# Kernel optimization log

Measured on AMD Instinct MI355X. Metric: run time of the kernel, lower is better.

The kernel has to match this reference:

```python
import jax, jax.numpy as jnp
import numpy as np


def _gcn(x, src, dst, W, b, n):
    # PyG GCNConv: out = D^-1/2 (A+I) D^-1/2 (x @ W) + b, deg includes self-loop
    xw = x @ W
    ones = jnp.ones(src.shape[0], x.dtype)
    deg = jax.ops.segment_sum(ones, dst, num_segments=n) + 1.0
    dinv = jax.lax.rsqrt(deg)
    norm = (dinv[src] * dinv[dst])[:, None]
    agg = jax.ops.segment_sum(xw[src] * norm, dst, num_segments=n)
    agg = agg + xw / deg[:, None]  # self-loop term: norm = 1/deg
    return agg + b


def _bn(x, g, b, m, v, eps=1e-5):
    # BatchNorm1d eval mode with running stats
    return (x - m) * jax.lax.rsqrt(v + eps) * g + b


def setup_inputs() -> dict:
    key = jax.random.key(0)
    ks = jax.random.split(key, 32)
    N, E, G, F, H, D, L, EM = 500000, 2500000, 10000, 64, 64, 128, 10, 160000
    s = 0.05
    inp = {
        'x': jax.random.normal(ks[0], (N, F), jnp.float32),
        'edge_index': jax.random.randint(ks[1], (2, E), 0, N),
        'batch': jnp.sort(jax.random.randint(ks[2], (N,), 0, G)),
        'macro_edges': jax.random.randint(ks[3], (2, EM), 0, G),
        'G': G,
        'W1': jax.random.normal(ks[4], (F, H)) * s, 'b1': jnp.zeros((H,)),
        'W2': jax.random.normal(ks[5], (H, H)) * s, 'b2': jnp.zeros((H,)),
        'FW1': jax.random.normal(ks[6], (H, D)) * s, 'Fb1': jnp.zeros((D,)),
        'FW2': jax.random.normal(ks[7], (D, L)) * s, 'Fb2': jnp.zeros((L,)),
        'MW1': jax.random.normal(ks[8], (D, D)) * s, 'mb1': jnp.zeros((D,)),
        'g1': jnp.ones((D,)), 'be1': jnp.zeros((D,)),
        'm1': jnp.zeros((D,)), 'v1': jnp.ones((D,)),
        'MW2': jax.random.normal(ks[9], (D, D)) * s, 'mb2': jnp.zeros((D,)),
        'g2': jnp.ones((D,)), 'be2': jnp.zeros((D,)),
        'm2': jnp.zeros((D,)), 'v2': jnp.ones((D,)),
        'MW3': jax.random.normal(ks[10], (D, L)) * s, 'mb3': jnp.zeros((L,)),
    }
    return inp


def reference(x, edge_index, batch, macro_edges, G,
              W1, b1, W2, b2, FW1, Fb1, FW2, Fb2,
              MW1, mb1, g1, be1, m1, v1,
              MW2, mb2, g2, be2, m2, v2,
              MW3, mb3):
    n = x.shape[0]
    src, dst = edge_index[0], edge_index[1]
    # SAGE (graph-level model), eval mode => dropout is identity
    h1 = jax.nn.relu(_gcn(x, src, dst, W1, b1, n))
    h2 = jax.nn.relu(_gcn(h1, src, dst, W2, b2, n))
    a1 = h2 @ FW1 + Fb1
    sums = jax.ops.segment_sum(a1, batch, num_segments=G)
    cnt = jax.ops.segment_sum(jnp.ones(n, x.dtype), batch, num_segments=G)
    loc = sums / jnp.maximum(cnt, 1.0)[:, None]        # [G, 128] graph embeddings
    ic = loc @ FW2 + Fb2                                # [G, L]
    # SuperMacroGCN over macro graph
    ms, md = macro_edges[0], macro_edges[1]
    z = jax.nn.relu(_bn(_gcn(loc, ms, md, MW1, mb1, G), g1, be1, m1, v1))
    z = jax.nn.relu(_bn(_gcn(z, ms, md, MW2, mb2, G), g2, be2, m2, v2))
    glob = z
    hc = _gcn(glob, ms, md, MW3, mb3, G)
    return (hc, ic, loc, glob, jnp.float32(0.0))
```

## Files before the change

kernel.cpp:

```cpp
#include <hip/hip_runtime.h>
#include <hip/hip_fp16.h>


typedef float nf4 __attribute__((ext_vector_type(4)));
typedef _Float16 v4h __attribute__((ext_vector_type(4)));
typedef float v4f __attribute__((ext_vector_type(4)));
struct __align__(8) h4 { __half2 a, b; };

__global__ void hist_kernel(const int* __restrict__ dst, int* __restrict__ hist, int E) {
    int e = blockIdx.x * blockDim.x + threadIdx.x;
    if (e < E) atomicAdd(&hist[dst[e]], 1);
}

__global__ void finalize_deg(const int* __restrict__ hist, float* __restrict__ dinv,
                             float* __restrict__ drecip, int n) {
    int i = blockIdx.x * blockDim.x + threadIdx.x;
    if (i < n) {
        float c = (float)hist[i] + 1.0f;
        dinv[i]   = rsqrtf(c);
        drecip[i] = 1.0f / c;
    }
}

__global__ __launch_bounds__(256) void scan1(const int* __restrict__ cnt, int* __restrict__ pre,
                                             int* __restrict__ bsum, int n) {
    __shared__ int s[256];
    int base = blockIdx.x * 1024;
    int t = threadIdx.x;
    int v[4];
    int loc = 0;
#pragma unroll
    for (int j = 0; j < 4; j++) {
        int i = base + t * 4 + j;
        v[j] = (i < n) ? cnt[i] : 0;
        loc += v[j];
    }
    s[t] = loc;
    __syncthreads();
    for (int off = 1; off < 256; off <<= 1) {
        int x = (t >= off) ? s[t - off] : 0;
        __syncthreads();
        s[t] += x;
        __syncthreads();
    }
    int run = s[t] - loc;
    if (t == 255) bsum[blockIdx.x] = s[255];
#pragma unroll
    for (int j = 0; j < 4; j++) {
        int i = base + t * 4 + j;
        if (i < n) pre[i] = run;
        run += v[j];
    }
}

__global__ __launch_bounds__(512) void scan2(int* __restrict__ bsum, int nb) {
    __shared__ int s[512];
    int t = threadIdx.x;
    int v = (t < nb) ? bsum[t] : 0;
    s[t] = v;
    __syncthreads();
    for (int off = 1; off < 512; off <<= 1) {
        int x = (t >= off) ? s[t - off] : 0;
        __syncthreads();
        s[t] += x;
        __syncthreads();
    }
    if (t < nb) bsum[t] = s[t] - v;
}

__global__ void scan3(int* __restrict__ pre, const int* __restrict__ bsum,
                      int* __restrict__ cursor, int n, int E) {
    int i = blockIdx.x * blockDim.x + threadIdx.x;
    if (i < n) {
        int v = pre[i] + bsum[i >> 10];
        pre[i] = v;
        cursor[i] = v;
    }
    if (i == 0) pre[n] = E;
}

__global__ __launch_bounds__(256) void scatter_xcd(const int* __restrict__ src,
                                                   const int* __restrict__ dst,
                                                   int* __restrict__ cursor,
                                                   int* __restrict__ col,
                                                   int E, int per_chunk, int npx) {
    int bucket = blockIdx.x & 7;
    int chunk  = blockIdx.x >> 3;
    int lo = bucket * npx;
    int hi = lo + npx;
    int e0 = chunk * per_chunk;
    int e1 = min(e0 + per_chunk, E);
    for (int e = e0 + threadIdx.x; e < e1; e += 256) {
        int d = dst[e];
        if (d < lo || d >= hi) continue;
        int p = atomicAdd(&cursor[d], 1);
        col[p] = src[e];
    }
}

__global__ void scatter_kernel(const int* __restrict__ src, const int* __restrict__ dst,
                               int* __restrict__ cursor, int* __restrict__ col, int E) {
    int e = blockIdx.x * blockDim.x + threadIdx.x;
    if (e >= E) return;
    int p = atomicAdd(&cursor[dst[e]], 1);
    col[p] = src[e];
}

__global__ __launch_bounds__(256) void csr_agg_bn128(const int* __restrict__ rowptr,
                                                     const int* __restrict__ col,
                                                     const float* __restrict__ A,
                                                     const float* __restrict__ bias,
                                                     const float* __restrict__ dinv,
                                                     const float* __restrict__ gam,
                                                     const float* __restrict__ bet,
                                                     const float* __restrict__ mean,
                                                     const float* __restrict__ var,
                                                     float* __restrict__ Z, int N) {
    constexpr int F = 128, TPN = 32, NPB = 8;
    int node = blockIdx.x * NPB + threadIdx.x / TPN;
    int lane = threadIdx.x % TPN;
    if (node >= N) return;
    int c = lane * 4;
    float4 acc = *(const float4*)&A[(size_t)node * F + c];
    int e0 = rowptr[node], e1 = rowptr[node + 1];
    int e = e0;
    for (; e + 4 <= e1; e += 4) {
        int s0 = col[e + 0], s1 = col[e + 1], s2 = col[e + 2], s3 = col[e + 3];
        float4 v0 = *(const float4*)&A[(size_t)s0 * F + c];
        float4 v1 = *(const float4*)&A[(size_t)s1 * F + c];
        float4 v2 = *(const float4*)&A[(size_t)s2 * F + c];
        float4 v3 = *(const float4*)&A[(size_t)s3 * F + c];
        acc.x += v0.x + v1.x + v2.x + v3.x;
        acc.y += v0.y + v1.y + v2.y + v3.y;
        acc.z += v0.z + v1.z + v2.z + v3.z;
        acc.w += v0.w + v1.w + v2.w + v3.w;
    }
    for (; e < e1; e++) {
        int s = col[e];
        float4 v = *(const float4*)&A[(size_t)s * F + c];
        acc.x += v.x; acc.y += v.y; acc.z += v.z; acc.w += v.w;
    }
    float dv = dinv[node];
    float4 b4 = *(const float4*)&bias[c];
    float4 g4 = *(const float4*)&gam[c];
    float4 be4 = *(const float4*)&bet[c];
    float4 m4 = *(const float4*)&mean[c];
    float4 v4 = *(const float4*)&var[c];
    float4 o;
    o.x = fmaxf((acc.x * dv + b4.x - m4.x) * rsqrtf(v4.x + 1e-5f) * g4.x + be4.x, 0.f);
    o.y = fmaxf((acc.y * dv + b4.y - m4.y) * rsqrtf(v4.y + 1e-5f) * g4.y + be4.y, 0.f);
    o.z = fmaxf((acc.z * dv + b4.z - m4.z) * rsqrtf(v4.z + 1e-5f) * g4.z + be4.z, 0.f);
    o.w = fmaxf((acc.w * dv + b4.w - m4.w) * rsqrtf(v4.w + 1e-5f) * g4.w + be4.w, 0.f);
    *(float4*)&Z[(size_t)node * F + c] = o;
}

__global__ __launch_bounds__(256) void gemm_n64(const float* __restrict__ X,
                                                const float* __restrict__ W,
                                                const float* __restrict__ dinv,
                                                __half* __restrict__ XW, int N) {
    __shared__ float Xs[64][68];
    const int tid = threadIdx.x;
    const int tc = tid & 15;
    const int tr = tid >> 4;
    const int r0 = blockIdx.x * 64;

#pragma unroll
    for (int p = 0; p < 4; p++) {
        int row = p * 16 + (tid >> 4);
        int col = (tid & 15) * 4;
        float4 v = make_float4(0.f, 0.f, 0.f, 0.f);
        if (r0 + row < N) {
            nf4 nv = __builtin_nontemporal_load((const nf4*)&X[(size_t)(r0 + row) * 64 + col]);
            v = make_float4(nv.x, nv.y, nv.z, nv.w);
        }
        *(float4*)&Xs[row][col] = v;
    }
    __syncthreads();

    float acc[4][4];
#pragma unroll
    for (int i = 0; i < 4; i++)
#pragma unroll
        for (int j = 0; j < 4; j++) acc[i][j] = 0.f;

    const float* wp = W + tc * 4;
#pragma unroll 8
    for (int k = 0; k < 64; k++) {
        float4 wv = *(const float4*)&wp[k * 64];
        float x0 = Xs[tr * 4 + 0][k];
        float x1 = Xs[tr * 4 + 1][k];
        float x2 = Xs[tr * 4 + 2][k];
        float x3 = Xs[tr * 4 + 3][k];
        acc[0][0] += x0 * wv.x; acc[0][1] += x0 * wv.y; acc[0][2] += x0 * wv.z; acc[0][3] += x0 * wv.w;
        acc[1][0] += x1 * wv.x; acc[1][1] += x1 * wv.y; acc[1][2] += x1 * wv.z; acc[1][3] += x1 * wv.w;
        acc[2][0] += x2 * wv.x; acc[2][1] += x2 * wv.y; acc[2][2] += x2 * wv.z; acc[2][3] += x2 * wv.w;
        acc[3][0] += x3 * wv.x; acc[3][1] += x3 * wv.y; acc[3][2] += x3 * wv.z; acc[3][3] += x3 * wv.w;
    }

#pragma unroll
    for (int i = 0; i < 4; i++) {
        int row = r0 + tr * 4 + i;
        if (row >= N) continue;
        float dv = dinv[row];
        h4 o;
        o.a = __floats2half2_rn(acc[i][0] * dv, acc[i][1] * dv);
        o.b = __floats2half2_rn(acc[i][2] * dv, acc[i][3] * dv);
        *(h4*)&XW[(size_t)row * 64 + tc * 4] = o;
    }
}

__global__ __launch_bounds__(256) void gemm_agg_n64(const int* __restrict__ rowptr,
                                                    const int* __restrict__ col,
                                                    const __half* __restrict__ A,
                                                    const float* __restrict__ b_prev,
                                                    const float* __restrict__ W,
                                                    const float* __restrict__ dinv,
                                                    __half* __restrict__ XW, int N) {
    __shared__ _Float16 Xh[64][68];
    __shared__ _Float16 WhT[64][68];
    const int tid = threadIdx.x;
    const int r0 = blockIdx.x * 64;

    for (int i = tid; i < 4096; i += 256) {
        int k = i >> 6, c = i & 63;
        WhT[c][k] = (_Float16)W[i];
    }

#pragma unroll
    for (int p = 0; p < 4; p++) {
        int row = p * 16 + (tid >> 4);
        int node = r0 + row;
        int c = (tid & 15) * 4;
        float4 acc = make_float4(0.f, 0.f, 0.f, 0.f);
        if (node < N) {
            h4 sv = *(const h4*)&A[(size_t)node * 64 + c];
            float2 f0 = __half22float2(sv.a);
            float2 f1 = __half22float2(sv.b);
            acc = make_float4(f0.x, f0.y, f1.x, f1.y);
            int e0 = rowptr[node], e1 = rowptr[node + 1];
            int e = e0;
            for (; e + 4 <= e1; e += 4) {
                int s0 = col[e + 0], s1 = col[e + 1], s2 = col[e + 2], s3 = col[e + 3];
                h4 v0 = *(const h4*)&A[(size_t)s0 * 64 + c];
                h4 v1 = *(const h4*)&A[(size_t)s1 * 64 + c];
                h4 v2 = *(const h4*)&A[(size_t)s2 * 64 + c];
                h4 v3 = *(const h4*)&A[(size_t)s3 * 64 + c];
                float2 a0 = __half22float2(v0.a), b0 = __half22float2(v0.b);
                float2 a1 = __half22float2(v1.a), b1 = __half22float2(v1.b);
                float2 a2 = __half22float2(v2.a), b2 = __half22float2(v2.b);
                float2 a3 = __half22float2(v3.a), b3 = __half22float2(v3.b);
                acc.x += a0.x + a1.x + a2.x + a3.x;
                acc.y += a0.y + a1.y + a2.y + a3.y;
                acc.z += b0.x + b1.x + b2.x + b3.x;
                acc.w += b0.y + b1.y + b2.y + b3.y;
            }
            for (; e < e1; e++) {
                int s = col[e];
                h4 v = *(const h4*)&A[(size_t)s * 64 + c];
                float2 a = __half22float2(v.a), b = __half22float2(v.b);
                acc.x += a.x; acc.y += a.y; acc.z += b.x; acc.w += b.y;
            }
            float dv = dinv[node];
            float4 b4 = *(const float4*)&b_prev[c];
            acc.x = fmaxf(acc.x * dv + b4.x, 0.f);
            acc.y = fmaxf(acc.y * dv + b4.y, 0.f);
            acc.z = fmaxf(acc.z * dv + b4.z, 0.f);
            acc.w = fmaxf(acc.w * dv + b4.w, 0.f);
        }
        v4h o;
        o.x = (_Float16)acc.x; o.y = (_Float16)acc.y;
        o.z = (_Float16)acc.z; o.w = (_Float16)acc.w;
        *(v4h*)&Xh[row][c] = o;
    }
    __syncthreads();

    const int wv = tid >> 6;
    const int lane = tid & 63;
    const int lr = lane & 15;
    const int kg = lane >> 4;

    v4f acc0 = {0.f, 0.f, 0.f, 0.f};
    v4f acc1 = {0.f, 0.f, 0.f, 0.f};
    v4f acc2 = {0.f, 0.f, 0.f, 0.f};
    v4f acc3 = {0.f, 0.f, 0.f, 0.f};
#pragma unroll
    for (int s = 0; s < 4; s++) {
        v4h af = *(const v4h*)&Xh[wv * 16 + lr][s * 16 + kg * 4];
        v4h bf0 = *(const v4h*)&WhT[0 * 16 + lr][s * 16 + kg * 4];
        v4h bf1 = *(const v4h*)&WhT[1 * 16 + lr][s * 16 + kg * 4];
        v4h bf2 = *(const v4h*)&WhT[2 * 16 + lr][s * 16 + kg * 4];
        v4h bf3 = *(const v4h*)&WhT[3 * 16 + lr][s * 16 + kg * 4];
        acc0 = __builtin_amdgcn_mfma_f32_16x16x16f16(af, bf0, acc0, 0, 0, 0);
        acc1 = __builtin_amdgcn_mfma_f32_16x16x16f16(af, bf1, acc1, 0, 0, 0);
        acc2 = __builtin_amdgcn_mfma_f32_16x16x16f16(af, bf2, acc2, 0, 0, 0);
        acc3 = __builtin_amdgcn_mfma_f32_16x16x16f16(af, bf3, acc3, 0, 0, 0);
    }

#pragma unroll
    for (int j = 0; j < 4; j++) {
        int row = r0 + wv * 16 + kg * 4 + j;
        if (row >= N) continue;
        float dv = dinv[row];
        XW[(size_t)row * 64 +  0 + lr] = (__half)(acc0[j] * dv);
        XW[(size_t)row * 64 + 16 + lr] = (__half)(acc1[j] * dv);
        XW[(size_t)row * 64 + 32 + lr] = (__half)(acc2[j] * dv);
        XW[(size_t)row * 64 + 48 + lr] = (__half)(acc3[j] * dv);
    }
}

__global__ __launch_bounds__(128) void segmean_agg(const int* __restrict__ rowptr,
                                                   const int* __restrict__ col,
                                                   const __half* __restrict__ A2,
                                                   const float* __restrict__ b2,
                                                   const float* __restrict__ dinv,
                                                   const int* __restrict__ batch,
                                                   float* __restrict__ M,
                                                   float* __restrict__ bscale,
                                                   int N, int G) {
    int g = blockIdx.x * 2 + (threadIdx.x >> 6);
    if (g >= G) return;
    int lane = threadIdx.x & 15;
    int sub  = (threadIdx.x >> 4) & 3;
    int c = lane * 4;

    int lo = 0, hi = N;
    while (lo < hi) { int m = (lo + hi) >> 1; if (batch[m] < g) lo = m + 1; else hi = m; }
    int start = lo;
    hi = N;
    while (lo < hi) { int m = (lo + hi) >> 1; if (batch[m] < g + 1) lo = m + 1; else hi = m; }
    int end = lo;

    float4 b4 = *(const float4*)&b2[c];
    float4 msum = make_float4(0.f, 0.f, 0.f, 0.f);

    for (int node = start + sub; node < end; node += 4) {
        h4 sv = *(const h4*)&A2[(size_t)node * 64 + c];
        float2 f0 = __half22float2(sv.a);
        float2 f1 = __half22float2(sv.b);
        float4 acc = make_float4(f0.x, f0.y, f1.x, f1.y);
        int e0 = rowptr[node], e1 = rowptr[node + 1];
        int e = e0;
        for (; e + 4 <= e1; e += 4) {
            int s0 = col[e + 0], s1 = col[e + 1], s2 = col[e + 2], s3 = col[e + 3];
            h4 v0 = *(const h4*)&A2[(size_t)s0 * 64 + c];
            h4 v1 = *(const h4*)&A2[(size_t)s1 * 64 + c];
            h4 v2 = *(const h4*)&A2[(size_t)s2 * 64 + c];
            h4 v3 = *(const h4*)&A2[(size_t)s3 * 64 + c];
            float2 a0 = __half22float2(v0.a), q0 = __half22float2(v0.b);
            float2 a1 = __half22float2(v1.a), q1 = __half22float2(v1.b);
            float2 a2 = __half22float2(v2.a), q2 = __half22float2(v2.b);
            float2 a3 = __half22float2(v3.a), q3 = __half22float2(v3.b);
            acc.x += a0.x + a1.x + a2.x + a3.x;
            acc.y += a0.y + a1.y + a2.y + a3.y;
            acc.z += q0.x + q1.x + q2.x + q3.x;
            acc.w += q0.y + q1.y + q2.y + q3.y;
        }
        for (; e < e1; e++) {
            int s = col[e];
            h4 v = *(const h4*)&A2[(size_t)s * 64 + c];
            float2 a = __half22float2(v.a), q = __half22float2(v.b);
            acc.x += a.x; acc.y += a.y; acc.z += q.x; acc.w += q.y;
        }
        float dv = dinv[node];
        msum.x += fmaxf(acc.x * dv + b4.x, 0.f);
        msum.y += fmaxf(acc.y * dv + b4.y, 0.f);
        msum.z += fmaxf(acc.z * dv + b4.z, 0.f);
        msum.w += fmaxf(acc.w * dv + b4.w, 0.f);
    }

    msum.x += __shfl_xor(msum.x, 16); msum.y += __shfl_xor(msum.y, 16);
    msum.z += __shfl_xor(msum.z, 16); msum.w += __shfl_xor(msum.w, 16);
    msum.x += __shfl_xor(msum.x, 32); msum.y += __shfl_xor(msum.y, 32);
    msum.z += __shfl_xor(msum.z, 32); msum.w += __shfl_xor(msum.w, 32);

    int cnt = end - start;
    float inv = (cnt > 0) ? 1.f / (float)cnt : 0.f;
    if (sub == 0) {
        float4 o;
        o.x = msum.x * inv; o.y = msum.y * inv;
        o.z = msum.z * inv; o.w = msum.w * inv;
        *(float4*)&M[(size_t)g * 64 + c] = o;
        if (lane == 0) bscale[g] = (cnt > 0) ? 1.f : 0.f;
    }
}

__global__ __launch_bounds__(256) void loc_gemm(const float* __restrict__ M,
                                                const float* __restrict__ FW1,
                                                const float* __restrict__ Fb1,
                                                const float* __restrict__ bscale,
                                                float* __restrict__ loc, int G) {
    __shared__ float Xs[64][68];
    __shared__ float Ws[64][64];
    __shared__ float bs[64];
    const int tid = threadIdx.x;
    const int tc = tid & 15;
    const int tr = tid >> 4;
    const int r0 = blockIdx.x * 64;
    const int c0 = blockIdx.y * 64;

    for (int i = tid; i < 4096; i += 256)
        Ws[i >> 6][i & 63] = FW1[(size_t)(i >> 6) * 128 + c0 + (i & 63)];
    if (tid < 64) bs[tid] = Fb1[c0 + tid];
#pragma unroll
    for (int p = 0; p < 4; p++) {
        int row = p * 16 + (tid >> 4);
        int col = (tid & 15) * 4;
        float4 v = make_float4(0.f, 0.f, 0.f, 0.f);
        if (r0 + row < G) v = *(const float4*)&M[(size_t)(r0 + row) * 64 + col];
        *(float4*)&Xs[row][col] = v;
    }
    __syncthreads();

    float acc[4][4];
#pragma unroll
    for (int i = 0; i < 4; i++)
#pragma unroll
        for (int j = 0; j < 4; j++) acc[i][j] = 0.f;

#pragma unroll 8
    for (int k = 0; k < 64; k++) {
        float4 wv = *(const float4*)&Ws[k][tc * 4];
        float x0 = Xs[tr * 4 + 0][k];
        float x1 = Xs[tr * 4 + 1][k];
        float x2 = Xs[tr * 4 + 2][k];
        float x3 = Xs[tr * 4 + 3][k];
        acc[0][0] += x0 * wv.x; acc[0][1] += x0 * wv.y; acc[0][2] += x0 * wv.z; acc[0][3] += x0 * wv.w;
        acc[1][0] += x1 * wv.x; acc[1][1] += x1 * wv.y; acc[1][2] += x1 * wv.z; acc[1][3] += x1 * wv.w;
        acc[2][0] += x2 * wv.x; acc[2][1] += x2 * wv.y; acc[2][2] += x2 * wv.z; acc[2][3] += x2 * wv.w;
        acc[3][0] += x3 * wv.x; acc[3][1] += x3 * wv.y; acc[3][2] += x3 * wv.z; acc[3][3] += x3 * wv.w;
    }

#pragma unroll
    for (int i = 0; i < 4; i++) {
        int row = r0 + tr * 4 + i;
        if (row >= G) continue;
        float sc = bscale[row];
        float4 o;
        o.x = acc[i][0] + sc * bs[tc * 4 + 0];
        o.y = acc[i][1] + sc * bs[tc * 4 + 1];
        o.z = acc[i][2] + sc * bs[tc * 4 + 2];
        o.w = acc[i][3] + sc * bs[tc * 4 + 3];
        *(float4*)&loc[(size_t)row * 128 + c0 + tc * 4] = o;
    }
}

__global__ __launch_bounds__(256) void ic_kernel(const float* __restrict__ loc,
                                                 const float* __restrict__ FW2,
                                                 const float* __restrict__ Fb2,
                                                 float* __restrict__ ic,
                                                 float* __restrict__ scalar_out, int G) {
    __shared__ float Ws[1280];
    __shared__ float bs[10];
    for (int i = threadIdx.x; i < 1280; i += 256) Ws[i] = FW2[i];
    if (threadIdx.x < 10) bs[threadIdx.x] = Fb2[threadIdx.x];
    __syncthreads();
    int g = blockIdx.x * 256 + threadIdx.x;
    if (g == 0) scalar_out[0] = 0.f;
    if (g >= G) return;
    float acc[10];
#pragma unroll
    for (int j = 0; j < 10; j++) acc[j] = bs[j];
    const float* xr = loc + (size_t)g * 128;
    for (int k = 0; k < 128; k++) {
        float xv = xr[k];
#pragma unroll
        for (int j = 0; j < 10; j++) acc[j] += xv * Ws[k * 10 + j];
    }
    float* o = ic + (size_t)g * 10;
#pragma unroll
    for (int j = 0; j < 10; j++) o[j] = acc[j];
}

__global__ __launch_bounds__(256) void gemm_g128(const float* __restrict__ X,
                                                 const float* __restrict__ W,
                                                 const float* __restrict__ dinv,
                                                 float* __restrict__ ZW, int G) {
    __shared__ float Xs[64][68];
    __shared__ float Ws[64][64];
    const int tid = threadIdx.x;
    const int tc = tid & 15;
    const int tr = tid >> 4;
    const int r0 = blockIdx.x * 64;
    const int c0 = blockIdx.y * 64;

    float acc[4][4];
#pragma unroll
    for (int i = 0; i < 4; i++)
#pragma unroll
        for (int j = 0; j < 4; j++) acc[i][j] = 0.f;

    for (int kc = 0; kc < 2; kc++) {
        __syncthreads();
        for (int i = tid; i < 4096; i += 256)
            Ws[i >> 6][i & 63] = W[(size_t)(kc * 64 + (i >> 6)) * 128 + c0 + (i & 63)];
#pragma unroll
        for (int p = 0; p < 4; p++) {
            int row = p * 16 + (tid >> 4);
            int col = (tid & 15) * 4;
            float4 v = make_float4(0.f, 0.f, 0.f, 0.f);
            if (r0 + row < G) v = *(const float4*)&X[(size_t)(r0 + row) * 128 + kc * 64 + col];
            *(float4*)&Xs[row][col] = v;
        }
        __syncthreads();
#pragma unroll 8
        for (int k = 0; k < 64; k++) {
            float4 wv = *(const float4*)&Ws[k][tc * 4];
            float x0 = Xs[tr * 4 + 0][k];
            float x1 = Xs[tr * 4 + 1][k];
            float x2 = Xs[tr * 4 + 2][k];
            float x3 = Xs[tr * 4 + 3][k];
            acc[0][0] += x0 * wv.x; acc[0][1] += x0 * wv.y; acc[0][2] += x0 * wv.z; acc[0][3] += x0 * wv.w;
            acc[1][0] += x1 * wv.x; acc[1][1] += x1 * wv.y; acc[1][2] += x1 * wv.z; acc[1][3] += x1 * wv.w;
            acc[2][0] += x2 * wv.x; acc[2][1] += x2 * wv.y; acc[2][2] += x2 * wv.z; acc[2][3] += x2 * wv.w;
            acc[3][0] += x3 * wv.x; acc[3][1] += x3 * wv.y; acc[3][2] += x3 * wv.z; acc[3][3] += x3 * wv.w;
        }
    }

#pragma unroll
    for (int i = 0; i < 4; i++) {
        int row = r0 + tr * 4 + i;
        if (row >= G) continue;
        float dv = dinv[row];
        *(float4*)&ZW[(size_t)row * 128 + c0 + tc * 4] =
            make_float4(acc[i][0] * dv, acc[i][1] * dv, acc[i][2] * dv, acc[i][3] * dv);
    }
}

__global__ __launch_bounds__(256) void gemm_g10(const float* __restrict__ X,
                                                const float* __restrict__ W,
                                                const float* __restrict__ bias,
                                                const float* __restrict__ mdrecip,
                                                float* __restrict__ ZW,
                                                float* __restrict__ HC, int G) {
    __shared__ float Ws[1280];
    __shared__ float bs[10];
    for (int i = threadIdx.x; i < 1280; i += 256) Ws[i] = W[i];
    if (threadIdx.x < 10) bs[threadIdx.x] = bias[threadIdx.x];
    __syncthreads();
    int g = blockIdx.x * 256 + threadIdx.x;
    if (g >= G) return;
    float acc[10];
#pragma unroll
    for (int j = 0; j < 10; j++) acc[j] = 0.f;
    const float4* xr = (const float4*)(X + (size_t)g * 128);
#pragma unroll 4
    for (int k4 = 0; k4 < 32; k4++) {
        float4 v = xr[k4];
        float xv[4] = {v.x, v.y, v.z, v.w};
#pragma unroll
        for (int d = 0; d < 4; d++) {
            float xs = xv[d];
            int k = k4 * 4 + d;
#pragma unroll
            for (int j = 0; j < 10; j++) acc[j] += xs * Ws[k * 10 + j];
        }
    }
    float dr = mdrecip[g];
    float* zw = ZW + (size_t)g * 10;
    float* hc = HC + (size_t)g * 10;
#pragma unroll
    for (int j = 0; j < 10; j++) {
        zw[j] = acc[j];
        hc[j] = acc[j] * dr + bs[j];
    }
}

__global__ void edge_agg10(const int* __restrict__ ms, const int* __restrict__ md,
                           const float* __restrict__ mdinv, const float* __restrict__ ZW,
                           float* __restrict__ HC, int EM) {
    int e = blockIdx.x * blockDim.x + threadIdx.x;
    if (e >= EM) return;
    int s = ms[e], d = md[e];
    float w = mdinv[s] * mdinv[d];
    const float* zr = ZW + (size_t)s * 10;
    float* out = HC + (size_t)d * 10;
#pragma unroll
    for (int j = 0; j < 10; j++) atomicAdd(out + j, zr[j] * w);
}

extern "C" void kernel_launch(void* const* d_in, const int* in_sizes, int n_in,
                              void* d_out, int out_size, void* d_ws, size_t ws_size,
                              hipStream_t stream) {
    const float* x    = (const float*)d_in[0];
    const int*   ei   = (const int*)d_in[1];
    const int*   batch= (const int*)d_in[2];
    const int*   me   = (const int*)d_in[3];
    const float* W1   = (const float*)d_in[5];
    const float* b1   = (const float*)d_in[6];
    const float* W2   = (const float*)d_in[7];
    const float* b2   = (const float*)d_in[8];
    const float* FW1  = (const float*)d_in[9];
    const float* Fb1  = (const float*)d_in[10];
    const float* FW2  = (const float*)d_in[11];
    const float* Fb2  = (const float*)d_in[12];
    const float* MW1  = (const float*)d_in[13];
    const float* mb1  = (const float*)d_in[14];
    const float* g1   = (const float*)d_in[15];
    const float* be1  = (const float*)d_in[16];
    const float* m1   = (const float*)d_in[17];
    const float* v1   = (const float*)d_in[18];
    const float* MW2  = (const float*)d_in[19];
    const float* mb2  = (const float*)d_in[20];
    const float* g2   = (const float*)d_in[21];
    const float* be2  = (const float*)d_in[22];
    const float* m2   = (const float*)d_in[23];
    const float* v2   = (const float*)d_in[24];
    const float* MW3  = (const float*)d_in[25];
    const float* mb3  = (const float*)d_in[26];

    const int N  = in_sizes[0] / 64;
    const int E  = in_sizes[1] / 2;
    const int EM = in_sizes[3] / 2;
    const int G  = (out_size - 1) / 276;

    float* out    = (float*)d_out;
    float* hc     = out;
    float* ic     = out + (size_t)G * 10;
    float* loc    = out + (size_t)G * 20;
    float* glob   = out + (size_t)G * 20 + (size_t)G * 128;
    float* scalar = out + (size_t)G * 276;

    char*  ws  = (char*)d_ws;
    size_t off = 0;
    auto alloc = [&](size_t bytes) -> void* {
        void* p = (void*)(ws + off);
        off += (bytes + 255) & ~(size_t)255;
        return p;
    };
    int*    hist    = (int*)alloc((size_t)(N + 1) * 4);
    int*    rowptr  = (int*)alloc((size_t)(N + 1) * 4);
    int*    cursor  = (int*)alloc((size_t)N * 4);
    int*    bsum    = (int*)alloc(512 * 4);
    int*    col     = (int*)alloc((size_t)E * 4);
    float*  dinv    = (float*)alloc((size_t)N * 4);
    float*  drecip  = (float*)alloc((size_t)N * 4);
    int*    mhist   = (int*)alloc((size_t)(G + 1) * 4);
    int*    mrowptr = (int*)alloc((size_t)(G + 1) * 4);
    int*    mcursor = (int*)alloc((size_t)G * 4);
    int*    mbsum   = (int*)alloc(512 * 4);
    int*    mcol    = (int*)alloc((size_t)EM * 4);
    float*  mdinv   = (float*)alloc((size_t)G * 4);
    float*  mdrecip = (float*)alloc((size_t)G * 4);
    __half* A       = (__half*)alloc((size_t)N * 64 * 2);
    __half* A2      = (__half*)alloc((size_t)N * 64 * 2);
    float*  M       = (float*)alloc((size_t)G * 64 * 4);
    float*  bscale  = (float*)alloc((size_t)G * 4);
    float*  mzw     = (float*)alloc((size_t)G * 128 * 4);
    float*  z1      = (float*)alloc((size_t)G * 128 * 4);
    float*  zw3     = (float*)alloc((size_t)G * 10 * 4);
    (void)ws_size;

    const int* src = ei;
    const int* dst = ei + E;
    const int* ms  = me;
    const int* md  = me + EM;

    hipMemsetAsync(hist, 0, (size_t)(N + 1) * 4, stream);
    hipMemsetAsync(mhist, 0, (size_t)(G + 1) * 4, stream);
    hist_kernel<<<(E + 255) / 256, 256, 0, stream>>>(dst, hist, E);
    hist_kernel<<<(EM + 255) / 256, 256, 0, stream>>>(md, mhist, EM);
    finalize_deg<<<(N + 255) / 256, 256, 0, stream>>>(hist, dinv, drecip, N);
    finalize_deg<<<(G + 255) / 256, 256, 0, stream>>>(mhist, mdinv, mdrecip, G);

    const int nb1 = (N + 1023) / 1024;
    scan1<<<nb1, 256, 0, stream>>>(hist, rowptr, bsum, N);
    scan2<<<1, 512, 0, stream>>>(bsum, nb1);
    scan3<<<(N + 255) / 256, 256, 0, stream>>>(rowptr, bsum, cursor, N, E);
    const int nb2 = (G + 1023) / 1024;
    scan1<<<nb2, 256, 0, stream>>>(mhist, mrowptr, mbsum, G);
    scan2<<<1, 512, 0, stream>>>(mbsum, nb2);
    scan3<<<(G + 255) / 256, 256, 0, stream>>>(mrowptr, mbsum, mcursor, G, EM);

    {
        const int nchunks = 2048;
        const int per_chunk = (E + nchunks - 1) / nchunks;
        const int npx = (N + 7) / 8;
        scatter_xcd<<<nchunks * 8, 256, 0, stream>>>(src, dst, cursor, col, E, per_chunk, npx);
    }
    scatter_kernel<<<(EM + 255) / 256, 256, 0, stream>>>(ms, md, mcursor, mcol, EM);

    const int nblk = (N + 63) / 64;

    gemm_n64<<<nblk, 256, 0, stream>>>(x, W1, dinv, A, N);
    gemm_agg_n64<<<nblk, 256, 0, stream>>>(rowptr, col, A, b1, W2, dinv, A2, N);
    segmean_agg<<<(G + 1) / 2, 128, 0, stream>>>(rowptr, col, A2, b2, dinv, batch, M, bscale, N, G);
    {
        dim3 lg((G + 63) / 64, 2);
        loc_gemm<<<lg, 256, 0, stream>>>(M, FW1, Fb1, bscale, loc, G);
    }
    ic_kernel<<<(G + 255) / 256, 256, 0, stream>>>(loc, FW2, Fb2, ic, scalar, G);

    dim3 mg((G + 63) / 64, 2);

    gemm_g128<<<mg, 256, 0, stream>>>(loc, MW1, mdinv, mzw, G);
    csr_agg_bn128<<<(G * 32 + 255) / 256, 256, 0, stream>>>(mrowptr, mcol, mzw, mb1, mdinv,
                                                            g1, be1, m1, v1, z1, G);
    gemm_g128<<<mg, 256, 0, stream>>>(z1, MW2, mdinv, mzw, G);
    csr_agg_bn128<<<(G * 32 + 255) / 256, 256, 0, stream>>>(mrowptr, mcol, mzw, mb2, mdinv,
                                                            g2, be2, m2, v2, glob, G);

    gemm_g10<<<(G + 255) / 256, 256, 0, stream>>>(glob, MW3, mb3, mdrecip, zw3, hc, G);
    edge_agg10<<<(EM + 255) / 256, 256, 0, stream>>>(ms, md, mdinv, zw3, hc, EM);
}
```

Before: 723.8 us.

## Parallelize segment-mean over node tiles with shared-memory run reduction and atomics

The segment-mean aggregation used to give each graph to one block, with a binary search over batch and a serial loop over that graph's nodes. It now processes 64-node tiles per block and reduces runs of equal graph ids in shared memory. The partial sums, already scaled by a precomputed inverse count, go to M with atomics. Graph counts and bscale move to a new small kernel, and M is zeroed with a memset. This balances load across nodes instead of across graphs, at the cost of float atomics (non-deterministic summation order) and an extra memset and launch.

Result: faster. 705.9 us (median of 2 runs) (-2.5%).

```diff
diff --git a/kernel.cpp b/kernel.cpp
--- a/kernel.cpp
+++ b/kernel.cpp
@@ -20,6 +20,20 @@
         dinv[i]   = rsqrtf(c);
         drecip[i] = 1.0f / c;
     }
+}
+
+__global__ void gcnt_kernel(const int* __restrict__ batch, float* __restrict__ invc,
+                            float* __restrict__ bscale, int N, int G) {
+    int g = blockIdx.x * blockDim.x + threadIdx.x;
+    if (g >= G) return;
+    int lo = 0, hi = N;
+    while (lo < hi) { int m = (lo + hi) >> 1; if (batch[m] < g) lo = m + 1; else hi = m; }
+    int s = lo;
+    hi = N;
+    while (lo < hi) { int m = (lo + hi) >> 1; if (batch[m] < g + 1) lo = m + 1; else hi = m; }
+    int cnt = lo - s;
+    invc[g]   = (cnt > 0) ? 1.f / (float)cnt : 0.f;
+    bscale[g] = (cnt > 0) ? 1.f : 0.f;
 }
 
 __global__ __launch_bounds__(256) void scan1(const int* __restrict__ cnt, int* __restrict__ pre,
@@ -308,79 +322,80 @@
     }
 }
 
-__global__ __launch_bounds__(128) void segmean_agg(const int* __restrict__ rowptr,
+__global__ __launch_bounds__(256) void segmean_agg(const int* __restrict__ rowptr,
                                                    const int* __restrict__ col,
                                                    const __half* __restrict__ A2,
                                                    const float* __restrict__ b2,
                                                    const float* __restrict__ dinv,
                                                    const int* __restrict__ batch,
-                                                   float* __restrict__ M,
-                                                   float* __restrict__ bscale,
-                                                   int N, int G) {
-    int g = blockIdx.x * 2 + (threadIdx.x >> 6);
-    if (g >= G) return;
-    int lane = threadIdx.x & 15;
-    int sub  = (threadIdx.x >> 4) & 3;
-    int c = lane * 4;
-
-    int lo = 0, hi = N;
-    while (lo < hi) { int m = (lo + hi) >> 1; if (batch[m] < g) lo = m + 1; else hi = m; }
-    int start = lo;
-    hi = N;
-    while (lo < hi) { int m = (lo + hi) >> 1; if (batch[m] < g + 1) lo = m + 1; else hi = m; }
-    int end = lo;
-
-    float4 b4 = *(const float4*)&b2[c];
-    float4 msum = make_float4(0.f, 0.f, 0.f, 0.f);
-
-    for (int node = start + sub; node < end; node += 4) {
-        h4 sv = *(const h4*)&A2[(size_t)node * 64 + c];
-        float2 f0 = __half22float2(sv.a);
-        float2 f1 = __half22float2(sv.b);
-        float4 acc = make_float4(f0.x, f0.y, f1.x, f1.y);
-        int e0 = rowptr[node], e1 = rowptr[node + 1];
-        int e = e0;
-        for (; e + 4 <= e1; e += 4) {
-            int s0 = col[e + 0], s1 = col[e + 1], s2 = col[e + 2], s3 = col[e + 3];
-            h4 v0 = *(const h4*)&A2[(size_t)s0 * 64 + c];
-            h4 v1 = *(const h4*)&A2[(size_t)s1 * 64 + c];
-            h4 v2 = *(const h4*)&A2[(size_t)s2 * 64 + c];
-            h4 v3 = *(const h4*)&A2[(size_t)s3 * 64 + c];
-            float2 a0 = __half22float2(v0.a), q0 = __half22float2(v0.b);
-            float2 a1 = __half22float2(v1.a), q1 = __half22float2(v1.b);
-            float2 a2 = __half22float2(v2.a), q2 = __half22float2(v2.b);
-            float2 a3 = __half22float2(v3.a), q3 = __half22float2(v3.b);
-            acc.x += a0.x + a1.x + a2.x + a3.x;
-            acc.y += a0.y + a1.y + a2.y + a3.y;
-            acc.z += q0.x + q1.x + q2.x + q3.x;
-            acc.w += q0.y + q1.y + q2.y + q3.y;
+                                                   const float* __restrict__ invc,
+                                                   float* __restrict__ M, int N) {
+    __shared__ float Xs[64][68];
+    __shared__ int gb[64];
+    const int tid = threadIdx.x;
+    const int r0 = blockIdx.x * 64;
+
+    if (tid < 64) gb[tid] = (r0 + tid < N) ? batch[r0 + tid] : -1;
+
+#pragma unroll
+    for (int p = 0; p < 4; p++) {
+        int row = p * 16 + (tid >> 4);
+        int node = r0 + row;
+        int c = (tid & 15) * 4;
+        float4 acc = make_float4(0.f, 0.f, 0.f, 0.f);
+        if (node < N) {
+            h4 sv = *(const h4*)&A2[(size_t)node * 64 + c];
+            float2 f0 = __half22float2(sv.a);
+            float2 f1 = __half22float2(sv.b);
+            acc = make_float4(f0.x, f0.y, f1.x, f1.y);
+            int e0 = rowptr[node], e1 = rowptr[node + 1];
+            int e = e0;
+            for (; e + 4 <= e1; e += 4) {
+                int s0 = col[e + 0], s1 = col[e + 1], s2 = col[e + 2], s3 = col[e + 3];
+                h4 v0 = *(const h4*)&A2[(size_t)s0 * 64 + c];
+                h4 v1 = *(const h4*)&A2[(size_t)s1 * 64 + c];
+                h4 v2 = *(const h4*)&A2[(size_t)s2 * 64 + c];
+                h4 v3 = *(const h4*)&A2[(size_t)s3 * 64 + c];
+                float2 a0 = __half22float2(v0.a), q0 = __half22float2(v0.b);
+                float2 a1 = __half22float2(v1.a), q1 = __half22float2(v1.b);
+                float2 a2 = __half22float2(v2.a), q2 = __half22float2(v2.b);
+                float2 a3 = __half22float2(v3.a), q3 = __half22float2(v3.b);
+                acc.x += a0.x + a1.x + a2.x + a3.x;
+                acc.y += a0.y + a1.y + a2.y + a3.y;
+                acc.z += q0.x + q1.x + q2.x + q3.x;
+                acc.w += q0.y + q1.y + q2.y + q3.y;
+            }
+            for (; e < e1; e++) {
+                int s = col[e];
+                h4 v = *(const h4*)&A2[(size_t)s * 64 + c];
+                float2 a = __half22float2(v.a), q = __half22float2(v.b);
+                acc.x += a.x; acc.y += a.y; acc.z += q.x; acc.w += q.y;
+            }
+            float dv = dinv[node];
+            float4 b4 = *(const float4*)&b2[c];
+            acc.x = fmaxf(acc.x * dv + b4.x, 0.f);
+            acc.y = fmaxf(acc.y * dv + b4.y, 0.f);
+            acc.z = fmaxf(acc.z * dv + b4.z, 0.f);
+            acc.w = fmaxf(acc.w * dv + b4.w, 0.f);
         }
-        for (; e < e1; e++) {
-            int s = col[e];
-            h4 v = *(const h4*)&A2[(size_t)s * 64 + c];
-            float2 a = __half22float2(v.a), q = __half22float2(v.b);
-            acc.x += a.x; acc.y += a.y; acc.z += q.x; acc.w += q.y;
+        *(float4*)&Xs[row][c] = acc;
+    }
+    __syncthreads();
+
+    if (tid < 64) {
+        int t = tid;
+        float run = 0.f;
+        int curg = gb[0];
+        for (int r = 0; r < 64; r++) {
+            int g2 = gb[r];
+            if (g2 != curg) {
+                if (curg >= 0) atomicAdd(&M[(size_t)curg * 64 + t], run * invc[curg]);
+                run = 0.f;
+                curg = g2;
+            }
+            if (g2 >= 0) run += Xs[r][t];
         }
-        float dv = dinv[node];
-        msum.x += fmaxf(acc.x * dv + b4.x, 0.f);
-        msum.y += fmaxf(acc.y * dv + b4.y, 0.f);
-        msum.z += fmaxf(acc.z * dv + b4.z, 0.f);
-        msum.w += fmaxf(acc.w * dv + b4.w, 0.f);
-    }
-
-    msum.x += __shfl_xor(msum.x, 16); msum.y += __shfl_xor(msum.y, 16);
-    msum.z += __shfl_xor(msum.z, 16); msum.w += __shfl_xor(msum.w, 16);
-    msum.x += __shfl_xor(msum.x, 32); msum.y += __shfl_xor(msum.y, 32);
-    msum.z += __shfl_xor(msum.z, 32); msum.w += __shfl_xor(msum.w, 32);
-
-    int cnt = end - start;
-    float inv = (cnt > 0) ? 1.f / (float)cnt : 0.f;
-    if (sub == 0) {
-        float4 o;
-        o.x = msum.x * inv; o.y = msum.y * inv;
-        o.z = msum.z * inv; o.w = msum.w * inv;
-        *(float4*)&M[(size_t)g * 64 + c] = o;
-        if (lane == 0) bscale[g] = (cnt > 0) ? 1.f : 0.f;
+        if (curg >= 0) atomicAdd(&M[(size_t)curg * 64 + t], run * invc[curg]);
     }
 }
 
@@ -644,6 +659,7 @@
     __half* A       = (__half*)alloc((size_t)N * 64 * 2);
     __half* A2      = (__half*)alloc((size_t)N * 64 * 2);
     float*  M       = (float*)alloc((size_t)G * 64 * 4);
+    float*  invc    = (float*)alloc((size_t)G * 4);
     float*  bscale  = (float*)alloc((size_t)G * 4);
     float*  mzw     = (float*)alloc((size_t)G * 128 * 4);
     float*  z1      = (float*)alloc((size_t)G * 128 * 4);
@@ -657,10 +673,12 @@
 
     hipMemsetAsync(hist, 0, (size_t)(N + 1) * 4, stream);
     hipMemsetAsync(mhist, 0, (size_t)(G + 1) * 4, stream);
+    hipMemsetAsync(M, 0, (size_t)G * 64 * 4, stream);
     hist_kernel<<<(E + 255) / 256, 256, 0, stream>>>(dst, hist, E);
     hist_kernel<<<(EM + 255) / 256, 256, 0, stream>>>(md, mhist, EM);
     finalize_deg<<<(N + 255) / 256, 256, 0, stream>>>(hist, dinv, drecip, N);
     finalize_deg<<<(G + 255) / 256, 256, 0, stream>>>(mhist, mdinv, mdrecip, G);
+    gcnt_kernel<<<(G + 255) / 256, 256, 0, stream>>>(batch, invc, bscale, N, G);
 
     const int nb1 = (N + 1023) / 1024;
     scan1<<<nb1, 256, 0, stream>>>(hist, rowptr, bsum, N);
@@ -683,7 +701,7 @@
 
     gemm_n64<<<nblk, 256, 0, stream>>>(x, W1, dinv, A, N);
     gemm_agg_n64<<<nblk, 256, 0, stream>>>(rowptr, col, A, b1, W2, dinv, A2, N);
-    segmean_agg<<<(G + 1) / 2, 128, 0, stream>>>(rowptr, col, A2, b2, dinv, batch, M, bscale, N, G);
+    segmean_agg<<<nblk, 256, 0, stream>>>(rowptr, col, A2, b2, dinv, batch, invc, M, N);
     {
         dim3 lg((G + 63) / 64, 2);
         loc_gemm<<<lg, 256, 0, stream>>>(M, FW1, Fb1, bscale, loc, G);
```
